# Kernel optimization log

Measured on AMD Instinct MI355X. Metric: run time of the kernel, lower is better.

## Reference

```python
import jax, jax.numpy as jnp
import numpy as np

BLOCK = 16
WINDOW = 6
NSEG = BLOCK - WINDOW + 1  # 11
ACT_TH = 0.1
IMP_TH = 0.1


def _gauss_kernel(size=7, sigma=7.0 / 6):
    m = (size - 1) / 2.0
    y, x = np.mgrid[-m:m + 1, -m:m + 1]
    h = np.exp(-(x * x + y * y) / (2.0 * sigma * sigma))
    h[h < np.finfo(h.dtype).eps * h.max()] = 0
    h /= h.sum()
    return jnp.asarray(h, dtype=jnp.float32)


def _normalize_with_gauss(img):
    # MSCN normalization: (img - mu) / (std + 1), gaussian 7x7 sigma=7/6, replicate pad
    k = _gauss_kernel()[None, None]  # [1,1,7,7]
    pad = 3
    p = jnp.pad(img, ((0, 0), (0, 0), (pad, pad), (pad, pad)), mode='edge')
    conv = lambda z: jax.lax.conv_general_dilated(z, k, (1, 1), 'VALID')
    mu = conv(p)
    mu2 = conv(p * p)
    std = jnp.sqrt(jnp.abs(mu2 - mu * mu))
    return (img - mu) / (std + 1.0)


def _seg_std_min(edge):
    # edge: [..., 16]; sliding windows of length 6 at offsets 0..10 (matches segment_edge)
    segs = jnp.stack([edge[..., i:i + WINDOW] for i in range(NSEG)], axis=-2)  # [...,11,6]
    return jnp.min(jnp.std(segs, axis=-1, ddof=1), axis=-1)


def _piqe_core(x):
    B, C, H, W = x.shape
    img = jnp.round(255.0 * x / jnp.max(x.reshape(B, -1), axis=-1)[:, None, None, None])
    col_pad, row_pad = W % BLOCK, H % BLOCK
    img = jnp.pad(img, ((0, 0), (0, 0), (0, row_pad), (0, col_pad)), mode='symmetric')
    n = _normalize_with_gauss(img)

    nbh, nbw = H // BLOCK, W // BLOCK
    blk = n[:, 0].reshape(B, nbh, BLOCK, nbw, BLOCK).transpose(0, 1, 3, 2, 4)  # [B,nbh,nbw,16,16]

    block_var = jnp.var(blk, axis=(-2, -1), ddof=1)  # unbiased
    active = block_var > ACT_TH

    # noticeable distortion: any edge sliding-segment std below threshold
    edges = (blk[..., 0, :], blk[..., :, BLOCK - 1], blk[..., BLOCK - 1, :], blk[..., :, 0])
    impaired = jnp.zeros_like(active)
    for e in edges:
        impaired = impaired | (_seg_std_min(e) < IMP_TH)

    # noise criterion: center-surround deviation (faithful to original indexing:
    # center = columns 7,8; surround excludes columns 7 and 9)
    center = jnp.concatenate([blk[..., :, 7], blk[..., :, 8]], axis=-1)  # [...,32]
    sur_cols = jnp.array([0, 1, 2, 3, 4, 5, 6, 8, 10, 11, 12, 13, 14, 15])
    sur = blk[..., :, sur_cols].reshape(B, nbh, nbw, -1)  # [...,224]
    csd = jnp.std(center, axis=-1, ddof=1) / jnp.std(sur, axis=-1, ddof=1)
    csd = jnp.where(jnp.isnan(csd), 0.0, csd)
    sigma = jnp.sqrt(block_var)
    beta = jnp.abs(sigma - csd) / jnp.maximum(sigma, csd)
    wnc = sigma > 2.0 * beta

    contrib = active * (impaired * (1.0 - block_var) + wnc * block_var)
    nhsa = jnp.sum(active, axis=(1, 2))
    score = (jnp.sum(contrib, axis=(1, 2)) + 1.0) / (1.0 + nhsa) * 100.0

    def expand(mb):  # [B,nbh,nbw] bool -> [B,1,H,W]
        return jnp.repeat(jnp.repeat(mb, BLOCK, axis=1), BLOCK, axis=2)[:, None]

    na_mask = expand(active & impaired)[..., :H, :W]
    noise_mask = expand(active & wnc)[..., :H, :W]
    act_mask = expand(active)[..., :H, :W]
    return score, na_mask, noise_mask, act_mask


def setup_inputs() -> dict:
    key = jax.random.key(0)
    x = jax.random.uniform(key, (8, 1, 2048, 2048), dtype=jnp.float32)
    return {"x": x}


def reference(x):
    score, na_mask, noise_mask, act_mask = _piqe_core(x)
    return score  # PIQE.forward returns results[0]
```

## Files before the change

### kernel.cpp

```cpp
#include <hip/hip_runtime.h>
#include <math.h>

#define IH 2048
#define IW 2048
#define NBATCH 8
#define TILE 64
#define HALO 3
#define SIW 70
#define SI 71
#define ACT_TH 0.1f
#define IMP_TH 0.1f

#define G0 0.0125602013f
#define G1 0.0788279697f
#define G2 0.2372960895f
#define G3 0.3426314790f

__device__ __forceinline__ float fsqrt_f(float x) { return __builtin_amdgcn_sqrtf(x); }
__device__ __forceinline__ float frcp_f(float x)  { return __builtin_amdgcn_rcpf(x); }

__global__ __launch_bounds__(256) void batch_max_kernel(
    const float* __restrict__ x, unsigned int* __restrict__ maxbits)
{
    const int b = blockIdx.y;
    const float4* p = (const float4*)(x + (size_t)b * (size_t)(IH * IW));
    const int n4 = IH * IW / 4;
    float m = 0.0f;
    for (int i = blockIdx.x * blockDim.x + threadIdx.x; i < n4;
         i += gridDim.x * blockDim.x) {
        float4 v = p[i];
        m = fmaxf(m, fmaxf(fmaxf(v.x, v.y), fmaxf(v.z, v.w)));
    }
#pragma unroll
    for (int s = 1; s < 64; s <<= 1) m = fmaxf(m, __shfl_xor(m, s));
    __shared__ float sm[4];
    const int lane = threadIdx.x & 63, wv = threadIdx.x >> 6;
    if (lane == 0) sm[wv] = m;
    __syncthreads();
    if (threadIdx.x == 0) {
        m = fmaxf(fmaxf(sm[0], sm[1]), fmaxf(sm[2], sm[3]));
        atomicMax(&maxbits[b], __float_as_uint(m));
    }
}

__global__ __launch_bounds__(256, 4) void piqe_main_kernel(
    const float* __restrict__ x, const unsigned int* __restrict__ maxbits,
    float* __restrict__ contrib_sum, unsigned int* __restrict__ nhsa)
{
    __shared__ float s_img[SIW * SI];
    __shared__ float s_c;
    __shared__ unsigned int s_a;

    const int tid = threadIdx.x;
    const int b = blockIdx.z;
    const int ox = blockIdx.x * TILE;
    const int oy = blockIdx.y * TILE;
    const float* img0 = x + (size_t)b * (size_t)(IH * IW);
    const float scale = 255.0f / __uint_as_float(maxbits[b]);

    if (tid == 0) { s_c = 0.0f; s_a = 0u; }

    for (int i = tid; i < SIW * SIW; i += 256) {
        int r = i / SIW, c = i - r * SIW;
        int gy = oy + r - HALO; gy = max(0, min(IH - 1, gy));
        int gx = ox + c - HALO; gx = max(0, min(IW - 1, gx));
        s_img[r * SI + c] = rintf(img0[(size_t)gy * IW + gx] * scale);
    }
    __syncthreads();

    const float gk[7] = {G0, G1, G2, G3, G2, G1, G0};

    const int cc = tid & 63;
    const int gg = tid >> 6;
    const int r0 = gg * 16;
    const float* bp = &s_img[r0 * SI + cc];

    float hm[7], h2[7], pv[4], nv[16];
#pragma unroll
    for (int j = 0; j < 22; ++j) {
        float m = 0.0f, m2 = 0.0f, ctr = 0.0f;
#pragma unroll
        for (int k = 0; k < 7; ++k) {
            float v = bp[j * SI + k];
            if (k == 3) ctr = v;
            m = fmaf(gk[k], v, m);
            m2 = fmaf(gk[k] * v, v, m2);
        }
        hm[j % 7] = m;
        h2[j % 7] = m2;
        if (j >= 3 && j <= 18) pv[(j - 3) & 3] = ctr;
        if (j >= 6) {
            const int r = j - 6;
            float vm = 0.0f, vm2 = 0.0f;
#pragma unroll
            for (int k = 0; k < 7; ++k) {
                vm = fmaf(gk[k], hm[(r + k) % 7], vm);
                vm2 = fmaf(gk[k], h2[(r + k) % 7], vm2);
            }
            float sd = fsqrt_f(fabsf(vm2 - vm * vm));
            nv[r] = (pv[r & 3] - vm) * frcp_f(sd + 1.0f);
        }
    }
    __syncthreads();

    {
        float* wp = &s_img[(r0 + HALO) * SI + (cc + HALO)];
#pragma unroll
        for (int r = 0; r < 16; ++r) wp[r * SI] = nv[r];
    }
    __syncthreads();

    const int lane = tid & 63;
    const int wv = tid >> 6;
    const int blk = wv * 4 + (lane >> 4);
    const int L = lane & 15;
    const int bi = blk >> 2, bj = blk & 3;
    const float* np0 = &s_img[(HALO + bi * 16) * SI + (HALO + bj * 16)];

    float rv[16];
    float s1 = 0.0f, s2 = 0.0f;
#pragma unroll
    for (int k = 0; k < 16; ++k) {
        float v = np0[L * SI + k];
        rv[k] = v;
        s1 += v;
        s2 += v * v;
    }
    float c1 = rv[7] + rv[8];
    float c2 = rv[7] * rv[7] + rv[8] * rv[8];
    float u1 = s1 - rv[7] - rv[9];
    float u2 = s2 - rv[7] * rv[7] - rv[9] * rv[9];

    float minstd = __builtin_inff();
    if (L < 4) {
        int offs, stp;
        if (L == 0)      { offs = 0;       stp = 1; }
        else if (L == 1) { offs = 15 * SI; stp = 1; }
        else if (L == 2) { offs = 0;       stp = SI; }
        else             { offs = 15;      stp = SI; }
        float e[16];
#pragma unroll
        for (int k = 0; k < 16; ++k) e[k] = np0[offs + k * stp];
        float w1 = 0.0f, w2 = 0.0f;
#pragma unroll
        for (int k = 0; k < 6; ++k) { w1 += e[k]; w2 += e[k] * e[k]; }
#pragma unroll
        for (int i = 0; i < 11; ++i) {
            float var = (w2 - w1 * w1 * (1.0f / 6.0f)) * (1.0f / 5.0f);
            minstd = fminf(minstd, fsqrt_f(fmaxf(var, 0.0f)));
            if (i < 10) {
                w1 += e[i + 6] - e[i];
                w2 += e[i + 6] * e[i + 6] - e[i] * e[i];
            }
        }
    }

#pragma unroll
    for (int m = 1; m < 16; m <<= 1) {
        s1 += __shfl_xor(s1, m);
        s2 += __shfl_xor(s2, m);
        c1 += __shfl_xor(c1, m);
        c2 += __shfl_xor(c2, m);
        u1 += __shfl_xor(u1, m);
        u2 += __shfl_xor(u2, m);
        minstd = fminf(minstd, __shfl_xor(minstd, m));
    }

    if (L == 0) {
        float bv = fmaxf((s2 - s1 * s1 * (1.0f / 256.0f)) * (1.0f / 255.0f), 0.0f);
        bool active = bv > ACT_TH;
        float cstd = fsqrt_f(fmaxf((c2 - c1 * c1 * (1.0f / 32.0f)) * (1.0f / 31.0f), 0.0f));
        float sstd = fsqrt_f(fmaxf((u2 - u1 * u1 * (1.0f / 224.0f)) * (1.0f / 223.0f), 0.0f));
        float csd = cstd * frcp_f(sstd);
        if (csd != csd) csd = 0.0f;
        float sigma = fsqrt_f(bv);
        float beta = fabsf(sigma - csd) * frcp_f(fmaxf(sigma, csd));
        bool wnc = sigma > 2.0f * beta;
        bool impaired = minstd < IMP_TH;
        if (active) {
            float contrib = (impaired ? (1.0f - bv) : 0.0f) + (wnc ? bv : 0.0f);
            atomicAdd(&s_c, contrib);
            atomicAdd(&s_a, 1u);
        }
    }
    __syncthreads();
    if (tid == 0) {
        atomicAdd(&contrib_sum[b], s_c);
        atomicAdd(&nhsa[b], s_a);
    }
}

__global__ void piqe_finish_kernel(const float* __restrict__ contrib_sum,
                                   const unsigned int* __restrict__ nhsa,
                                   float* __restrict__ out)
{
    int b = threadIdx.x;
    if (b < NBATCH)
        out[b] = (contrib_sum[b] + 1.0f) / (1.0f + (float)nhsa[b]) * 100.0f;
}

extern "C" void kernel_launch(void* const* d_in, const int* in_sizes, int n_in,
                              void* d_out, int out_size, void* d_ws, size_t ws_size,
                              hipStream_t stream)
{
    const float* x = (const float*)d_in[0];
    float* out = (float*)d_out;

    unsigned int* maxbits = (unsigned int*)d_ws;
    float* contrib = (float*)((char*)d_ws + 32);
    unsigned int* nhsa = (unsigned int*)((char*)d_ws + 64);

    hipMemsetAsync(d_ws, 0, 96, stream);
    batch_max_kernel<<<dim3(128, NBATCH), 256, 0, stream>>>(x, maxbits);
    piqe_main_kernel<<<dim3(IW / TILE, IH / TILE, NBATCH), 256, 0, stream>>>(
        x, maxbits, contrib, nhsa);
    piqe_finish_kernel<<<1, 64, 0, stream>>>(contrib, nhsa, out);
}
```

Baseline: 327.5 us.

## Compute Gaussian normalization as 4x4 register tiles with swizzled float4 LDS

```diff
diff --git a/kernel.cpp b/kernel.cpp
--- a/kernel.cpp
+++ b/kernel.cpp
@@ -6,8 +6,8 @@
 #define NBATCH 8
 #define TILE 64
 #define HALO 3
-#define SIW 70
-#define SI 71
+#define SROW 80
+#define NROW 68
 #define ACT_TH 0.1f
 #define IMP_TH 0.1f
 
@@ -18,6 +18,11 @@
 
 __device__ __forceinline__ float fsqrt_f(float x) { return __builtin_amdgcn_sqrtf(x); }
 __device__ __forceinline__ float frcp_f(float x)  { return __builtin_amdgcn_rcpf(x); }
+
+__device__ __forceinline__ int simg_ix(int r, int c) {
+    int m = (c >> 2) ^ ((r >> 2) & 3);
+    return r * SROW + (m << 2) + (c & 3);
+}
 
 __global__ __launch_bounds__(256) void batch_max_kernel(
     const float* __restrict__ x, unsigned int* __restrict__ maxbits)
@@ -47,7 +52,8 @@
     const float* __restrict__ x, const unsigned int* __restrict__ maxbits,
     float* __restrict__ contrib_sum, unsigned int* __restrict__ nhsa)
 {
-    __shared__ float s_img[SIW * SI];
+    __shared__ __align__(16) float s_img[70 * SROW];
+    __shared__ __align__(16) float s_nv[64 * NROW];
     __shared__ float s_c;
     __shared__ unsigned int s_a;
 
@@ -60,53 +66,96 @@
 
     if (tid == 0) { s_c = 0.0f; s_a = 0u; }
 
-    for (int i = tid; i < SIW * SIW; i += 256) {
-        int r = i / SIW, c = i - r * SIW;
-        int gy = oy + r - HALO; gy = max(0, min(IH - 1, gy));
-        int gx = ox + c - HALO; gx = max(0, min(IW - 1, gx));
-        s_img[r * SI + c] = rintf(img0[(size_t)gy * IW + gx] * scale);
+    if (ox != 0 && oy != 0 && ox != IW - TILE && oy != IH - TILE) {
+        const float* base = img0 + (size_t)(oy - HALO) * IW + (ox - HALO);
+        for (int i = tid; i < 70 * 70; i += 256) {
+            int r = i / 70, c = i - r * 70;
+            s_img[simg_ix(r, c)] = rintf(base[r * IW + c] * scale);
+        }
+    } else {
+        for (int i = tid; i < 70 * 70; i += 256) {
+            int r = i / 70, c = i - r * 70;
+            int gy = oy + r - HALO; gy = max(0, min(IH - 1, gy));
+            int gx = ox + c - HALO; gx = max(0, min(IW - 1, gx));
+            s_img[simg_ix(r, c)] = rintf(img0[(size_t)gy * IW + gx] * scale);
+        }
     }
     __syncthreads();
 
     const float gk[7] = {G0, G1, G2, G3, G2, G1, G0};
-
-    const int cc = tid & 63;
-    const int gg = tid >> 6;
-    const int r0 = gg * 16;
-    const float* bp = &s_img[r0 * SI + cc];
-
-    float hm[7], h2[7], pv[4], nv[16];
-#pragma unroll
-    for (int j = 0; j < 22; ++j) {
-        float m = 0.0f, m2 = 0.0f, ctr = 0.0f;
-#pragma unroll
-        for (int k = 0; k < 7; ++k) {
-            float v = bp[j * SI + k];
-            if (k == 3) ctr = v;
-            m = fmaf(gk[k], v, m);
-            m2 = fmaf(gk[k] * v, v, m2);
-        }
-        hm[j % 7] = m;
-        h2[j % 7] = m2;
-        if (j >= 3 && j <= 18) pv[(j - 3) & 3] = ctr;
-        if (j >= 6) {
-            const int r = j - 6;
-            float vm = 0.0f, vm2 = 0.0f;
+    const int q = tid & 15;
+    const int g = tid >> 4;
+
+    float vm[4][4], vm2[4][4], pv[4][4];
+#pragma unroll
+    for (int r = 0; r < 4; ++r)
+#pragma unroll
+        for (int c = 0; c < 4; ++c) { vm[r][c] = 0.0f; vm2[r][c] = 0.0f; }
+
+#pragma unroll
+    for (int jj = 0; jj < 10; ++jj) {
+        const int row = 4 * g + jj;
+        const int s = (row >> 2) & 3;
+        const float4* rp = (const float4*)&s_img[row * SROW];
+        float4 A = rp[q ^ s];
+        float4 B = rp[(q + 1) ^ s];
+        float4 C = rp[(q + 2) ^ s];
+        float w[12] = {A.x, A.y, A.z, A.w, B.x, B.y, B.z, B.w,
+                       C.x, C.y, C.z, C.w};
+
+        float hm[4], h2[4];
+#pragma unroll
+        for (int c = 0; c < 4; ++c) {
+            float m = 0.0f, m2 = 0.0f;
 #pragma unroll
             for (int k = 0; k < 7; ++k) {
-                vm = fmaf(gk[k], hm[(r + k) % 7], vm);
-                vm2 = fmaf(gk[k], h2[(r + k) % 7], vm2);
-            }
-            float sd = fsqrt_f(fabsf(vm2 - vm * vm));
-            nv[r] = (pv[r & 3] - vm) * frcp_f(sd + 1.0f);
-        }
-    }
-    __syncthreads();
-
-    {
-        float* wp = &s_img[(r0 + HALO) * SI + (cc + HALO)];
-#pragma unroll
-        for (int r = 0; r < 16; ++r) wp[r * SI] = nv[r];
+                float v = w[c + k];
+                m = fmaf(gk[k], v, m);
+                m2 = fmaf(gk[k] * v, v, m2);
+            }
+            hm[c] = m; h2[c] = m2;
+        }
+        if (jj >= 3 && jj <= 6) {
+#pragma unroll
+            for (int c = 0; c < 4; ++c) pv[jj - 3][c] = w[c + 3];
+        }
+#pragma unroll
+        for (int r = 0; r < 4; ++r) {
+            const int k = jj - r;
+            if (k >= 0 && k < 7) {
+#pragma unroll
+                for (int c = 0; c < 4; ++c) {
+                    vm[r][c]  = fmaf(gk[k], hm[c], vm[r][c]);
+                    vm2[r][c] = fmaf(gk[k], h2[c], vm2[r][c]);
+                }
+            }
+        }
+        if (jj >= 6) {
+            const int r = jj - 6;
+            float o0, o1, o2, o3;
+            {
+                float m = vm[r][0];
+                float sd = fsqrt_f(fabsf(vm2[r][0] - m * m));
+                o0 = (pv[r][0] - m) * frcp_f(sd + 1.0f);
+            }
+            {
+                float m = vm[r][1];
+                float sd = fsqrt_f(fabsf(vm2[r][1] - m * m));
+                o1 = (pv[r][1] - m) * frcp_f(sd + 1.0f);
+            }
+            {
+                float m = vm[r][2];
+                float sd = fsqrt_f(fabsf(vm2[r][2] - m * m));
+                o2 = (pv[r][2] - m) * frcp_f(sd + 1.0f);
+            }
+            {
+                float m = vm[r][3];
+                float sd = fsqrt_f(fabsf(vm2[r][3] - m * m));
+                o3 = (pv[r][3] - m) * frcp_f(sd + 1.0f);
+            }
+            *(float4*)&s_nv[(4 * g + r) * NROW + 4 * q] =
+                make_float4(o0, o1, o2, o3);
+        }
     }
     __syncthreads();
 
@@ -115,14 +164,21 @@
     const int blk = wv * 4 + (lane >> 4);
     const int L = lane & 15;
     const int bi = blk >> 2, bj = blk & 3;
-    const float* np0 = &s_img[(HALO + bi * 16) * SI + (HALO + bj * 16)];
+    const float* np0 = &s_nv[(bi * 16) * NROW + bj * 16];
 
     float rv[16];
+    {
+        const float4* rp4 = (const float4*)(np0 + L * NROW);
+        float4 r0 = rp4[0], r1 = rp4[1], r2 = rp4[2], r3 = rp4[3];
+        rv[0] = r0.x; rv[1] = r0.y; rv[2]  = r0.z; rv[3]  = r0.w;
+        rv[4] = r1.x; rv[5] = r1.y; rv[6]  = r1.z; rv[7]  = r1.w;
+        rv[8] = r2.x; rv[9] = r2.y; rv[10] = r2.z; rv[11] = r2.w;
+        rv[12] = r3.x; rv[13] = r3.y; rv[14] = r3.z; rv[15] = r3.w;
+    }
     float s1 = 0.0f, s2 = 0.0f;
 #pragma unroll
     for (int k = 0; k < 16; ++k) {
-        float v = np0[L * SI + k];
-        rv[k] = v;
+        float v = rv[k];
         s1 += v;
         s2 += v * v;
     }
@@ -134,10 +190,10 @@
     float minstd = __builtin_inff();
     if (L < 4) {
         int offs, stp;
-        if (L == 0)      { offs = 0;       stp = 1; }
-        else if (L == 1) { offs = 15 * SI; stp = 1; }
-        else if (L == 2) { offs = 0;       stp = SI; }
-        else             { offs = 15;      stp = SI; }
+        if (L == 0)      { offs = 0;         stp = 1; }
+        else if (L == 1) { offs = 15 * NROW; stp = 1; }
+        else if (L == 2) { offs = 0;         stp = NROW; }
+        else             { offs = 15;        stp = NROW; }
         float e[16];
 #pragma unroll
         for (int k = 0; k < 16; ++k) e[k] = np0[offs + k * stp];
```

New measurement: 334.1 us. 2.0% more time.

## Persistent tile loop, fused finish via ticket, fast interior halo load

Applied to the files above, without the earlier changes.

```diff
diff --git a/kernel.cpp b/kernel.cpp
--- a/kernel.cpp
+++ b/kernel.cpp
@@ -11,6 +11,9 @@
 #define ACT_TH 0.1f
 #define IMP_TH 0.1f
 
+#define TGRID 2048
+#define NTILES 8192
+
 #define G0 0.0125602013f
 #define G1 0.0788279697f
 #define G2 0.2372960895f
@@ -19,57 +22,34 @@
 __device__ __forceinline__ float fsqrt_f(float x) { return __builtin_amdgcn_sqrtf(x); }
 __device__ __forceinline__ float frcp_f(float x)  { return __builtin_amdgcn_rcpf(x); }
 
-__global__ __launch_bounds__(256) void batch_max_kernel(
-    const float* __restrict__ x, unsigned int* __restrict__ maxbits)
-{
-    const int b = blockIdx.y;
-    const float4* p = (const float4*)(x + (size_t)b * (size_t)(IH * IW));
-    const int n4 = IH * IW / 4;
-    float m = 0.0f;
-    for (int i = blockIdx.x * blockDim.x + threadIdx.x; i < n4;
-         i += gridDim.x * blockDim.x) {
-        float4 v = p[i];
-        m = fmaxf(m, fmaxf(fmaxf(v.x, v.y), fmaxf(v.z, v.w)));
-    }
-#pragma unroll
-    for (int s = 1; s < 64; s <<= 1) m = fmaxf(m, __shfl_xor(m, s));
-    __shared__ float sm[4];
-    const int lane = threadIdx.x & 63, wv = threadIdx.x >> 6;
-    if (lane == 0) sm[wv] = m;
-    __syncthreads();
-    if (threadIdx.x == 0) {
-        m = fmaxf(fmaxf(sm[0], sm[1]), fmaxf(sm[2], sm[3]));
-        atomicMax(&maxbits[b], __float_as_uint(m));
-    }
-}
-
-__global__ __launch_bounds__(256, 4) void piqe_main_kernel(
-    const float* __restrict__ x, const unsigned int* __restrict__ maxbits,
-    float* __restrict__ contrib_sum, unsigned int* __restrict__ nhsa)
+__device__ __forceinline__ void piqe_tile(
+    const float* __restrict__ img0, float scale,
+    float* __restrict__ contrib_sum, unsigned int* __restrict__ nhsa,
+    int b, int ox, int oy, int tid)
 {
     __shared__ float s_img[SIW * SI];
     __shared__ float s_c;
     __shared__ unsigned int s_a;
 
-    const int tid = threadIdx.x;
-    const int b = blockIdx.z;
-    const int ox = blockIdx.x * TILE;
-    const int oy = blockIdx.y * TILE;
-    const float* img0 = x + (size_t)b * (size_t)(IH * IW);
-    const float scale = 255.0f / __uint_as_float(maxbits[b]);
-
     if (tid == 0) { s_c = 0.0f; s_a = 0u; }
 
-    for (int i = tid; i < SIW * SIW; i += 256) {
-        int r = i / SIW, c = i - r * SIW;
-        int gy = oy + r - HALO; gy = max(0, min(IH - 1, gy));
-        int gx = ox + c - HALO; gx = max(0, min(IW - 1, gx));
-        s_img[r * SI + c] = rintf(img0[(size_t)gy * IW + gx] * scale);
+    if (ox != 0 && oy != 0 && ox != IW - TILE && oy != IH - TILE) {
+        const float* base = img0 + (size_t)(oy - HALO) * IW + (ox - HALO);
+        for (int i = tid; i < SIW * SIW; i += 256) {
+            int r = i / SIW, c = i - r * SIW;
+            s_img[r * SI + c] = rintf(base[r * IW + c] * scale);
+        }
+    } else {
+        for (int i = tid; i < SIW * SIW; i += 256) {
+            int r = i / SIW, c = i - r * SIW;
+            int gy = oy + r - HALO; gy = max(0, min(IH - 1, gy));
+            int gx = ox + c - HALO; gx = max(0, min(IW - 1, gx));
+            s_img[r * SI + c] = rintf(img0[(size_t)gy * IW + gx] * scale);
+        }
     }
     __syncthreads();
 
     const float gk[7] = {G0, G1, G2, G3, G2, G1, G0};
-
     const int cc = tid & 63;
     const int gg = tid >> 6;
     const int r0 = gg * 16;
@@ -190,13 +170,62 @@
     }
 }
 
-__global__ void piqe_finish_kernel(const float* __restrict__ contrib_sum,
-                                   const unsigned int* __restrict__ nhsa,
-                                   float* __restrict__ out)
-{
-    int b = threadIdx.x;
-    if (b < NBATCH)
-        out[b] = (contrib_sum[b] + 1.0f) / (1.0f + (float)nhsa[b]) * 100.0f;
+__global__ __launch_bounds__(256) void batch_max_kernel(
+    const float* __restrict__ x, unsigned int* __restrict__ maxbits)
+{
+    const int b = blockIdx.y;
+    const float4* p = (const float4*)(x + (size_t)b * (size_t)(IH * IW));
+    const int n4 = IH * IW / 4;
+    float m = 0.0f;
+    for (int i = blockIdx.x * blockDim.x + threadIdx.x; i < n4;
+         i += gridDim.x * blockDim.x) {
+        float4 v = p[i];
+        m = fmaxf(m, fmaxf(fmaxf(v.x, v.y), fmaxf(v.z, v.w)));
+    }
+#pragma unroll
+    for (int s = 1; s < 64; s <<= 1) m = fmaxf(m, __shfl_xor(m, s));
+    __shared__ float sm[4];
+    const int lane = threadIdx.x & 63, wv = threadIdx.x >> 6;
+    if (lane == 0) sm[wv] = m;
+    __syncthreads();
+    if (threadIdx.x == 0) {
+        m = fmaxf(fmaxf(sm[0], sm[1]), fmaxf(sm[2], sm[3]));
+        atomicMax(&maxbits[b], __float_as_uint(m));
+    }
+}
+
+__global__ __launch_bounds__(256) void piqe_tiles_kernel(
+    const float* __restrict__ x, const unsigned int* __restrict__ maxbits,
+    float* __restrict__ contrib_sum, unsigned int* __restrict__ nhsa,
+    unsigned int* __restrict__ ticket, float* __restrict__ out)
+{
+    const int tid = threadIdx.x;
+
+#pragma unroll 1
+    for (int t = blockIdx.x; t < NTILES; t += TGRID) {
+        const int b = t >> 10;
+        const int tt = t & 1023;
+        const int oy = (tt >> 5) * TILE;
+        const int ox = (tt & 31) * TILE;
+        const float* img0 = x + (size_t)b * (size_t)(IH * IW);
+        const float scale = 255.0f / __uint_as_float(maxbits[b]);
+        piqe_tile(img0, scale, contrib_sum, nhsa, b, ox, oy, tid);
+    }
+
+    __shared__ unsigned int s_win;
+    if (tid == 0) {
+        unsigned int tk = __hip_atomic_fetch_add(
+            ticket, 1u, __ATOMIC_ACQ_REL, __HIP_MEMORY_SCOPE_AGENT);
+        s_win = (tk == (unsigned int)(TGRID - 1)) ? 1u : 0u;
+    }
+    __syncthreads();
+    if (s_win && tid < NBATCH) {
+        float c = __hip_atomic_load(&contrib_sum[tid], __ATOMIC_RELAXED,
+                                    __HIP_MEMORY_SCOPE_AGENT);
+        unsigned int a = __hip_atomic_load(&nhsa[tid], __ATOMIC_RELAXED,
+                                           __HIP_MEMORY_SCOPE_AGENT);
+        out[tid] = (c + 1.0f) / (1.0f + (float)a) * 100.0f;
+    }
 }
 
 extern "C" void kernel_launch(void* const* d_in, const int* in_sizes, int n_in,
@@ -209,10 +238,10 @@
     unsigned int* maxbits = (unsigned int*)d_ws;
     float* contrib = (float*)((char*)d_ws + 32);
     unsigned int* nhsa = (unsigned int*)((char*)d_ws + 64);
-
-    hipMemsetAsync(d_ws, 0, 96, stream);
-    batch_max_kernel<<<dim3(128, NBATCH), 256, 0, stream>>>(x, maxbits);
-    piqe_main_kernel<<<dim3(IW / TILE, IH / TILE, NBATCH), 256, 0, stream>>>(
-        x, maxbits, contrib, nhsa);
-    piqe_finish_kernel<<<1, 64, 0, stream>>>(contrib, nhsa, out);
-}
+    unsigned int* ticket = (unsigned int*)((char*)d_ws + 96);
+
+    hipMemsetAsync(d_ws, 0, 128, stream);
+    batch_max_kernel<<<dim3(256, NBATCH), 256, 0, stream>>>(x, maxbits);
+    piqe_tiles_kernel<<<dim3(TGRID), 256, 0, stream>>>(
+        x, maxbits, contrib, nhsa, ticket, out);
+}
```

New measurement: 368.8 us. +12.6%, slower.

## Vectorize tile loads and shared-memory reads, widen max-reduction grid

Applied to the files above, without the earlier changes.

```diff
diff --git a/kernel.cpp b/kernel.cpp
--- a/kernel.cpp
+++ b/kernel.cpp
@@ -7,7 +7,7 @@
 #define TILE 64
 #define HALO 3
 #define SIW 70
-#define SI 71
+#define SI 72
 #define ACT_TH 0.1f
 #define IMP_TH 0.1f
 
@@ -19,15 +19,17 @@
 __device__ __forceinline__ float fsqrt_f(float x) { return __builtin_amdgcn_sqrtf(x); }
 __device__ __forceinline__ float frcp_f(float x)  { return __builtin_amdgcn_rcpf(x); }
 
+#define MAXBLK 256
+#define MAXSTRIDE (MAXBLK * 256)
 __global__ __launch_bounds__(256) void batch_max_kernel(
     const float* __restrict__ x, unsigned int* __restrict__ maxbits)
 {
     const int b = blockIdx.y;
     const float4* p = (const float4*)(x + (size_t)b * (size_t)(IH * IW));
-    const int n4 = IH * IW / 4;
     float m = 0.0f;
-    for (int i = blockIdx.x * blockDim.x + threadIdx.x; i < n4;
-         i += gridDim.x * blockDim.x) {
+    int i = blockIdx.x * 256 + threadIdx.x;
+#pragma unroll
+    for (int it = 0; it < (IH * IW / 4) / MAXSTRIDE; ++it, i += MAXSTRIDE) {
         float4 v = p[i];
         m = fmaxf(m, fmaxf(fmaxf(v.x, v.y), fmaxf(v.z, v.w)));
     }
@@ -43,11 +45,11 @@
     }
 }
 
-__global__ __launch_bounds__(256, 4) void piqe_main_kernel(
+__global__ __launch_bounds__(256) void piqe_main_kernel(
     const float* __restrict__ x, const unsigned int* __restrict__ maxbits,
     float* __restrict__ contrib_sum, unsigned int* __restrict__ nhsa)
 {
-    __shared__ float s_img[SIW * SI];
+    __shared__ __align__(16) float s_img[SIW * SI];
     __shared__ float s_c;
     __shared__ unsigned int s_a;
 
@@ -60,20 +62,34 @@
 
     if (tid == 0) { s_c = 0.0f; s_a = 0u; }
 
-    for (int i = tid; i < SIW * SIW; i += 256) {
-        int r = i / SIW, c = i - r * SIW;
-        int gy = oy + r - HALO; gy = max(0, min(IH - 1, gy));
-        int gx = ox + c - HALO; gx = max(0, min(IW - 1, gx));
-        s_img[r * SI + c] = rintf(img0[(size_t)gy * IW + gx] * scale);
+    if (ox != 0 && oy != 0 && ox != IW - TILE && oy != IH - TILE) {
+        const float* base4 = img0 + (size_t)(oy - HALO) * IW + (ox - 4);
+        for (int u = tid; u < SIW * 18; u += 256) {
+            int r = u / 18;
+            int s = u - r * 18;
+            float4 q = *(const float4*)(base4 + (size_t)r * IW + 4 * s);
+            float4 o;
+            o.x = rintf(q.x * scale);
+            o.y = rintf(q.y * scale);
+            o.z = rintf(q.z * scale);
+            o.w = rintf(q.w * scale);
+            *(float4*)&s_img[r * SI + 4 * s] = o;
+        }
+    } else {
+        for (int i = tid; i < SIW * SIW; i += 256) {
+            int r = i / SIW, c = i - r * SIW;
+            int gy = oy + r - HALO; gy = max(0, min(IH - 1, gy));
+            int gx = ox + c - HALO; gx = max(0, min(IW - 1, gx));
+            s_img[r * SI + c + 1] = rintf(img0[(size_t)gy * IW + gx] * scale);
+        }
     }
     __syncthreads();
 
     const float gk[7] = {G0, G1, G2, G3, G2, G1, G0};
-
     const int cc = tid & 63;
     const int gg = tid >> 6;
     const int r0 = gg * 16;
-    const float* bp = &s_img[r0 * SI + cc];
+    const float* bp = &s_img[r0 * SI + cc + 1];
 
     float hm[7], h2[7], pv[4], nv[16];
 #pragma unroll
@@ -104,7 +120,7 @@
     __syncthreads();
 
     {
-        float* wp = &s_img[(r0 + HALO) * SI + (cc + HALO)];
+        float* wp = &s_img[(r0 + HALO) * SI + cc + HALO + 1];
 #pragma unroll
         for (int r = 0; r < 16; ++r) wp[r * SI] = nv[r];
     }
@@ -115,14 +131,21 @@
     const int blk = wv * 4 + (lane >> 4);
     const int L = lane & 15;
     const int bi = blk >> 2, bj = blk & 3;
-    const float* np0 = &s_img[(HALO + bi * 16) * SI + (HALO + bj * 16)];
+    const float* np0 = &s_img[(HALO + bi * 16) * SI + (HALO + 1 + bj * 16)];
 
     float rv[16];
+    {
+        const float4* rp4 = (const float4*)(np0 + L * SI);
+        float4 q0 = rp4[0], q1 = rp4[1], q2 = rp4[2], q3 = rp4[3];
+        rv[0] = q0.x; rv[1] = q0.y; rv[2]  = q0.z; rv[3]  = q0.w;
+        rv[4] = q1.x; rv[5] = q1.y; rv[6]  = q1.z; rv[7]  = q1.w;
+        rv[8] = q2.x; rv[9] = q2.y; rv[10] = q2.z; rv[11] = q2.w;
+        rv[12] = q3.x; rv[13] = q3.y; rv[14] = q3.z; rv[15] = q3.w;
+    }
     float s1 = 0.0f, s2 = 0.0f;
 #pragma unroll
     for (int k = 0; k < 16; ++k) {
-        float v = np0[L * SI + k];
-        rv[k] = v;
+        float v = rv[k];
         s1 += v;
         s2 += v * v;
     }
@@ -211,7 +234,7 @@
     unsigned int* nhsa = (unsigned int*)((char*)d_ws + 64);
 
     hipMemsetAsync(d_ws, 0, 96, stream);
-    batch_max_kernel<<<dim3(128, NBATCH), 256, 0, stream>>>(x, maxbits);
+    batch_max_kernel<<<dim3(MAXBLK, NBATCH), 256, 0, stream>>>(x, maxbits);
     piqe_main_kernel<<<dim3(IW / TILE, IH / TILE, NBATCH), 256, 0, stream>>>(
         x, maxbits, contrib, nhsa);
     piqe_finish_kernel<<<1, 64, 0, stream>>>(contrib, nhsa, out);
```

After: 317.9 us. 2.9% less time.
